# Kernel tuning notes

Measured on AMD Instinct MI355X. Metric: run time of the kernel, lower is better.

The kernel has to match this reference:

```python
import jax, jax.numpy as jnp
import numpy as np

B, N_TOTAL = 4096, 512
DIMS = {"RT": (8, 8, 16), "OB": (8, 8, 16), "RS": (8, 8, 16), "TG": (16, 16, 32)}


def _branch(obs, W, b, dq, dk):
    # obs: [B, n, 2]; fused QKV projection then self-attention + mean pool
    P = obs @ W + b                              # [B, n, dq+dk+dv]
    Q, K, V = P[..., :dq], P[..., dq:dq + dk], P[..., dq + dk:]
    scores = jnp.einsum('bqd,bkd->bqk', Q, K) / (dk ** 0.5)
    A = jax.nn.softmax(scores, axis=-1)
    return jnp.mean(jnp.einsum('bqk,bkv->bqv', A, V), axis=1)  # [B, dv]


def setup_inputs() -> dict:
    key = jax.random.key(0)
    ks = jax.random.split(key, 16)
    inp = {"state": jax.random.normal(ks[0], (B, N_TOTAL, 3), jnp.float32),
           "num_rt": 128, "num_ob": 128, "num_rs": 128, "num_tg": 128}
    i = 1
    for name, (dq, dk, dv) in DIMS.items():
        inp[f"W_{name}"] = 0.1 * jax.random.normal(ks[i], (2, dq + dk + dv), jnp.float32)
        inp[f"b_{name}"] = jnp.zeros((dq + dk + dv,), jnp.float32)
        i += 1
    dcat = sum(d[2] for d in DIMS.values())  # 64
    inp["W1"] = 0.1 * jax.random.normal(ks[i], (dcat, 256), jnp.float32)
    inp["b1"] = jnp.zeros((256,), jnp.float32)
    inp["W2"] = 0.1 * jax.random.normal(ks[i + 1], (256, 256), jnp.float32)
    inp["b2"] = jnp.zeros((256,), jnp.float32)
    inp["W3"] = 0.01 * jax.random.normal(ks[i + 2], (256, 1), jnp.float32)
    inp["b3"] = jnp.zeros((1,), jnp.float32)
    return inp


def reference(state, num_rt, num_ob, num_rs, num_tg,
              W_RT, b_RT, W_OB, b_OB, W_RS, b_RS, W_TG, b_TG,
              W1, b1, W2, b2, W3, b3):
    o0, o1 = 0, num_rt
    o2, o3 = o1 + num_ob, o1 + num_ob + num_rs
    o4 = o3 + num_tg
    h_rt = _branch(state[:, o0:o1, 0:2], W_RT, b_RT, *DIMS["RT"][:2])
    h_ob = _branch(state[:, o1:o2, 0:2], W_OB, b_OB, *DIMS["OB"][:2])
    h_rs = _branch(state[:, o2:o3, 0:2], W_RS, b_RS, *DIMS["RS"][:2])
    h_tg = _branch(state[:, o3:o4, 0:2], W_TG, b_TG, *DIMS["TG"][:2])
    h = jnp.concatenate([h_rt, h_ob, h_rs, h_tg], axis=1)  # [B, 64]
    h = jnp.tanh(h @ W1 + b1)
    h = jnp.tanh(h @ W2 + b2)
    return h @ W3 + b3  # [B, 1]
```

## Files before the change

kernel.cpp:

```cpp
#include <hip/hip_runtime.h>

#define LOG2E 1.44269504088896340736f

typedef float v2f __attribute__((ext_vector_type(2)));

__device__ __forceinline__ float fexp2(float x){
#if __has_builtin(__builtin_amdgcn_exp2f)
  return __builtin_amdgcn_exp2f(x);
#else
  return exp2f(x);
#endif
}
__device__ __forceinline__ float frcp(float x){
#if __has_builtin(__builtin_amdgcn_rcpf)
  return __builtin_amdgcn_rcpf(x);
#else
  return 1.0f/x;
#endif
}
__device__ __forceinline__ float tanh_fast(float x){
  float e = fexp2(x * (2.0f*LOG2E));
  return 1.0f - 2.0f*frcp(e + 1.0f);
}
__device__ __forceinline__ float4 fma4(float s, float4 w, float4 a){
  a.x = fmaf(s,w.x,a.x); a.y = fmaf(s,w.y,a.y);
  a.z = fmaf(s,w.z,a.z); a.w = fmaf(s,w.w,a.w);
  return a;
}
__device__ __forceinline__ v2f vfma2(v2f a, v2f b, v2f c){
#if __has_builtin(__builtin_elementwise_fma)
  return __builtin_elementwise_fma(a,b,c);
#else
  v2f r; r.x=fmaf(a.x,b.x,c.x); r.y=fmaf(a.y,b.y,c.y); return r;
#endif
}

template<int DQ, int DV>
__device__ __forceinline__ void branch_run(
    const float* __restrict__ state, int b, int n0,
    const float* __restrict__ W, const float* __restrict__ bias,
    float4* __restrict__ su4, float* __restrict__ sy,
    float* __restrict__ sH, int lane)
{
  const int D = 4*DQ;
  const float qs = LOG2E * (DQ==8 ? 0.35355339059327373f : 0.25f);

  const float* sp = state + ((size_t)b*512 + (size_t)(n0 + lane))*3;
  float x0 = sp[0],   y0 = sp[1];
  float x1 = sp[192], y1 = sp[193];

  float M00=0,M01=0,M02=0,M10=0,M11=0,M12=0,M20=0,M21=0,M22=0;
  #pragma unroll
  for (int d=0; d<DQ; ++d) {
    float aq0 = W[d], aq1 = W[D+d], aq2 = bias[d];
    float ak0 = W[DQ+d], ak1 = W[D+DQ+d], ak2 = bias[DQ+d];
    M00 = fmaf(aq0,ak0,M00); M01 = fmaf(aq0,ak1,M01); M02 = fmaf(aq0,ak2,M02);
    M10 = fmaf(aq1,ak0,M10); M11 = fmaf(aq1,ak1,M11); M12 = fmaf(aq1,ak2,M12);
    M20 = fmaf(aq2,ak0,M20); M21 = fmaf(aq2,ak1,M21); M22 = fmaf(aq2,ak2,M22);
  }
  M00*=qs; M01*=qs; M02*=qs; M10*=qs; M11*=qs; M12*=qs; M20*=qs; M21*=qs; M22*=qs;

  float4 uA, uB;
  uA.x = fmaf(M00,x0, fmaf(M01,y0, M02));
  uA.y = fmaf(M10,x0, fmaf(M11,y0, M12));
  uA.z = fmaf(M20,x0, fmaf(M21,y0, M22));
  uA.w = x0;
  uB.x = fmaf(M00,x1, fmaf(M01,y1, M02));
  uB.y = fmaf(M10,x1, fmaf(M11,y1, M12));
  uB.z = fmaf(M20,x1, fmaf(M21,y1, M22));
  uB.w = x1;
  su4[lane]    = uA;  sy[lane]    = y0;
  su4[lane+64] = uB;  sy[lane+64] = y1;
  __syncthreads();

  v2f X; X.x=x0; X.y=x1;
  v2f Y; Y.x=y0; Y.y=y1;
  v2f E={0.f,0.f}, Ex={0.f,0.f}, Ey={0.f,0.f};
  const float4* syc = (const float4*)sy;
  #pragma unroll 4
  for (int k4=0; k4<32; ++k4) {
    float4 yv = syc[k4];
    #pragma unroll
    for (int j=0; j<4; ++j) {
      float4 u = su4[4*k4+j];
      float yk = (j==0)?yv.x : (j==1)?yv.y : (j==2)?yv.z : yv.w;
      v2f ux; ux.x=u.x; ux.y=u.x;
      v2f uy; uy.x=u.y; uy.y=u.y;
      v2f uz; uz.x=u.z; uz.y=u.z;
      v2f s = vfma2(X, ux, vfma2(Y, uy, uz));
      v2f e; e.x = fexp2(s.x); e.y = fexp2(s.y);
      E += e;
      v2f xk2; xk2.x=u.w; xk2.y=u.w;
      v2f yk2; yk2.x=yk;  yk2.y=yk;
      Ex = vfma2(e, xk2, Ex);
      Ey = vfma2(e, yk2, Ey);
    }
  }
  float r0 = frcp(E.x), r1 = frcp(E.y);
  float gx = fmaf(Ex.x,r0, Ex.y*r1);
  float gy = fmaf(Ey.x,r0, Ey.y*r1);
  #pragma unroll
  for (int m=1; m<64; m<<=1) {
    gx += __shfl_xor(gx, m, 64);
    gy += __shfl_xor(gy, m, 64);
  }
  gx *= 0.0078125f;
  gy *= 0.0078125f;
  if (lane < DV) {
    float wv0 = W[2*DQ+lane], wv1 = W[D+2*DQ+lane], vb = bias[2*DQ+lane];
    sH[lane] = fmaf(gx, wv0, fmaf(gy, wv1, vb));
  }
}

__global__ __launch_bounds__(256)
void attn_kernel(const float* __restrict__ state,
    const float* __restrict__ W_RT, const float* __restrict__ b_RT,
    const float* __restrict__ W_OB, const float* __restrict__ b_OB,
    const float* __restrict__ W_RS, const float* __restrict__ b_RS,
    const float* __restrict__ W_TG, const float* __restrict__ b_TG,
    float* __restrict__ hbuf)
{
  __shared__ float4 su4[4*128];
  __shared__ float  sy[4*128] __attribute__((aligned(16)));
  __shared__ float  sH[80];
  const int b    = blockIdx.x;
  const int wave = threadIdx.x >> 6;
  const int lane = threadIdx.x & 63;

  const float* W;  const float* bb;
  if      (wave == 0) { W = W_RT; bb = b_RT; }
  else if (wave == 1) { W = W_OB; bb = b_OB; }
  else if (wave == 2) { W = W_RS; bb = b_RS; }
  else                { W = W_TG; bb = b_TG; }
  const int n0 = wave * 128;
  float4* u4   = su4 + wave * 128;
  float*  yy   = sy  + wave * 128;
  float*  hOut = sH + wave * 16;

  if (wave < 3) branch_run<8 ,16>(state, b, n0, W, bb, u4, yy, hOut, lane);
  else          branch_run<16,32>(state, b, n0, W, bb, u4, yy, hOut, lane);
  __syncthreads();
  if (threadIdx.x < 80) hbuf[(size_t)b*80 + threadIdx.x] = sH[threadIdx.x];
}

__global__ __launch_bounds__(256)
void mlp_kernel(const float* __restrict__ hbuf,
    const float* __restrict__ W1, const float* __restrict__ b1,
    const float* __restrict__ W2, const float* __restrict__ b2,
    const float* __restrict__ W3, const float* __restrict__ b3,
    float* __restrict__ out)
{
  __shared__ float sHin[8][84];
  __shared__ float sH1[8][260];
  __shared__ float sRed[4][8];
  const int t  = threadIdx.x;
  const int b0 = blockIdx.x * 8;
  const int q  = t >> 2;
  const int rg = t & 3;
  const int r0 = 2*rg, r1 = r0 + 1;
  const int wave = t >> 6;

  for (int i = t; i < 8*80; i += 256) sHin[i/80][i%80] = hbuf[(size_t)b0*80 + i];
  __syncthreads();

  const float4* W1v = (const float4*)W1;
  const float4* W2v = (const float4*)W2;

  float4 acc0 = ((const float4*)b1)[q];
  float4 acc1 = acc0;
  float4 wb[4][4];
  #pragma unroll
  for (int p=0; p<4; ++p)
    #pragma unroll
    for (int jj=0; jj<4; ++jj) wb[p][jj] = W1v[(size_t)(4*p+jj)*64 + q];
  #pragma unroll 4
  for (int i4 = 0; i4 < 16; ++i4) {
    float4 h0 = *(const float4*)&sHin[r0][i4*4];
    float4 h1 = *(const float4*)&sHin[r1][i4*4];
    float4 w0=wb[i4&3][0], w1=wb[i4&3][1], w2=wb[i4&3][2], w3=wb[i4&3][3];
    #pragma unroll
    for (int jj=0; jj<4; ++jj) wb[i4&3][jj] = W1v[(size_t)((i4+4)*4+jj)*64 + q];
    acc0 = fma4(h0.x,w0, fma4(h0.y,w1, fma4(h0.z,w2, fma4(h0.w,w3, acc0))));
    acc1 = fma4(h1.x,w0, fma4(h1.y,w1, fma4(h1.z,w2, fma4(h1.w,w3, acc1))));
  }
  #pragma unroll
  for (int i4 = 16; i4 < 20; ++i4) {
    float4 h0 = *(const float4*)&sHin[r0][i4*4];
    float4 h1 = *(const float4*)&sHin[r1][i4*4];
    float4 w0=wb[i4&3][0], w1=wb[i4&3][1], w2=wb[i4&3][2], w3=wb[i4&3][3];
    acc0 = fma4(h0.x,w0, fma4(h0.y,w1, fma4(h0.z,w2, fma4(h0.w,w3, acc0))));
    acc1 = fma4(h1.x,w0, fma4(h1.y,w1, fma4(h1.z,w2, fma4(h1.w,w3, acc1))));
  }
  {
    float4 o0, o1;
    o0.x=tanh_fast(acc0.x); o0.y=tanh_fast(acc0.y); o0.z=tanh_fast(acc0.z); o0.w=tanh_fast(acc0.w);
    o1.x=tanh_fast(acc1.x); o1.y=tanh_fast(acc1.y); o1.z=tanh_fast(acc1.z); o1.w=tanh_fast(acc1.w);
    *(float4*)&sH1[r0][4*q] = o0;
    *(float4*)&sH1[r1][4*q] = o1;
  }
  __syncthreads();

  float4 acc2_0 = ((const float4*)b2)[q];
  float4 acc2_1 = acc2_0;
  #pragma unroll
  for (int p=0; p<4; ++p)
    #pragma unroll
    for (int jj=0; jj<4; ++jj) wb[p][jj] = W2v[(size_t)(4*p+jj)*64 + q];
  #pragma unroll 4
  for (int i4 = 0; i4 < 60; ++i4) {
    float4 h0 = *(const float4*)&sH1[r0][i4*4];
    float4 h1 = *(const float4*)&sH1[r1][i4*4];
    float4 w0=wb[i4&3][0], w1=wb[i4&3][1], w2=wb[i4&3][2], w3=wb[i4&3][3];
    #pragma unroll
    for (int jj=0; jj<4; ++jj) wb[i4&3][jj] = W2v[(size_t)((i4+4)*4+jj)*64 + q];
    acc2_0 = fma4(h0.x,w0, fma4(h0.y,w1, fma4(h0.z,w2, fma4(h0.w,w3, acc2_0))));
    acc2_1 = fma4(h1.x,w0, fma4(h1.y,w1, fma4(h1.z,w2, fma4(h1.w,w3, acc2_1))));
  }
  #pragma unroll
  for (int i4 = 60; i4 < 64; ++i4) {
    float4 h0 = *(const float4*)&sH1[r0][i4*4];
    float4 h1 = *(const float4*)&sH1[r1][i4*4];
    float4 w0=wb[i4&3][0], w1=wb[i4&3][1], w2=wb[i4&3][2], w3=wb[i4&3][3];
    acc2_0 = fma4(h0.x,w0, fma4(h0.y,w1, fma4(h0.z,w2, fma4(h0.w,w3, acc2_0))));
    acc2_1 = fma4(h1.x,w0, fma4(h1.y,w1, fma4(h1.z,w2, fma4(h1.w,w3, acc2_1))));
  }

  float4 w3v = ((const float4*)W3)[q];
  float p0 = tanh_fast(acc2_0.x)*w3v.x + tanh_fast(acc2_0.y)*w3v.y
           + tanh_fast(acc2_0.z)*w3v.z + tanh_fast(acc2_0.w)*w3v.w;
  float p1 = tanh_fast(acc2_1.x)*w3v.x + tanh_fast(acc2_1.y)*w3v.y
           + tanh_fast(acc2_1.z)*w3v.z + tanh_fast(acc2_1.w)*w3v.w;
  #pragma unroll
  for (int m=4; m<64; m<<=1) {
    p0 += __shfl_xor(p0, m, 64);
    p1 += __shfl_xor(p1, m, 64);
  }
  if ((t & 63) == rg) { sRed[wave][r0] = p0; sRed[wave][r1] = p1; }
  __syncthreads();
  if (t < 8)
    out[b0 + t] = sRed[0][t] + sRed[1][t] + sRed[2][t] + sRed[3][t] + b3[0];
}

extern "C" void kernel_launch(void* const* d_in, const int* in_sizes, int n_in,
                              void* d_out, int out_size, void* d_ws, size_t ws_size,
                              hipStream_t stream) {
  const float* state = (const float*)d_in[0];
  const float* W_RT = (const float*)d_in[5];
  const float* b_RT = (const float*)d_in[6];
  const float* W_OB = (const float*)d_in[7];
  const float* b_OB = (const float*)d_in[8];
  const float* W_RS = (const float*)d_in[9];
  const float* b_RS = (const float*)d_in[10];
  const float* W_TG = (const float*)d_in[11];
  const float* b_TG = (const float*)d_in[12];
  const float* W1 = (const float*)d_in[13];
  const float* b1 = (const float*)d_in[14];
  const float* W2 = (const float*)d_in[15];
  const float* b2 = (const float*)d_in[16];
  const float* W3 = (const float*)d_in[17];
  const float* b3 = (const float*)d_in[18];

  float* hbuf = (float*)d_ws;

  attn_kernel<<<4096, 256, 0, stream>>>(state,
      W_RT, b_RT, W_OB, b_OB, W_RS, b_RS, W_TG, b_TG, hbuf);
  mlp_kernel<<<512, 256, 0, stream>>>(hbuf, W1, b1, W2, b2, W3, b3,
      (float*)d_out);
}
```

Measured before the change: 75.74 us.

## Batch four samples per attention block, pair keys in LDS, deepen MLP prefetch

The attention kernel now handles four consecutive batch rows per block, 1024 blocks instead of 4096. This amortizes the per-branch Q·K bilinear-form setup and the V-weight loads across rows. Keys are stored in LDS interleaved in pairs, so each packed two-wide FMA covers two keys for the same query, while each thread still handles its two queries. The MLP kernel gets a deeper 8-stage register prefetch of W2 and a min-2-blocks occupancy hint. The risks are fewer blocks to hide latency, extra barriers per row, and more register pressure from the larger prefetch buffer.

```diff
diff --git a/kernel.cpp b/kernel.cpp
--- a/kernel.cpp
+++ b/kernel.cpp
@@ -35,19 +35,16 @@
 #endif
 }
 
-template<int DQ, int DV>
-__device__ __forceinline__ void branch_run(
-    const float* __restrict__ state, int b, int n0,
+template<int DQ, int DV, int NB>
+__device__ __forceinline__ void branch_all(
+    const float* __restrict__ state, int b0, int n0,
     const float* __restrict__ W, const float* __restrict__ bias,
-    float4* __restrict__ su4, float* __restrict__ sy,
-    float* __restrict__ sH, int lane)
+    float* __restrict__ sA, float* __restrict__ sB, float* __restrict__ sYv,
+    float* __restrict__ sHbase, int hoff, float* __restrict__ hbuf,
+    int lane, int tix)
 {
   const int D = 4*DQ;
   const float qs = LOG2E * (DQ==8 ? 0.35355339059327373f : 0.25f);
-
-  const float* sp = state + ((size_t)b*512 + (size_t)(n0 + lane))*3;
-  float x0 = sp[0],   y0 = sp[1];
-  float x1 = sp[192], y1 = sp[193];
 
   float M00=0,M01=0,M02=0,M10=0,M11=0,M12=0,M20=0,M21=0,M22=0;
   #pragma unroll
@@ -60,55 +57,84 @@
   }
   M00*=qs; M01*=qs; M02*=qs; M10*=qs; M11*=qs; M12*=qs; M20*=qs; M21*=qs; M22*=qs;
 
-  float4 uA, uB;
-  uA.x = fmaf(M00,x0, fmaf(M01,y0, M02));
-  uA.y = fmaf(M10,x0, fmaf(M11,y0, M12));
-  uA.z = fmaf(M20,x0, fmaf(M21,y0, M22));
-  uA.w = x0;
-  uB.x = fmaf(M00,x1, fmaf(M01,y1, M02));
-  uB.y = fmaf(M10,x1, fmaf(M11,y1, M12));
-  uB.z = fmaf(M20,x1, fmaf(M21,y1, M22));
-  uB.w = x1;
-  su4[lane]    = uA;  sy[lane]    = y0;
-  su4[lane+64] = uB;  sy[lane+64] = y1;
-  __syncthreads();
-
-  v2f X; X.x=x0; X.y=x1;
-  v2f Y; Y.x=y0; Y.y=y1;
-  v2f E={0.f,0.f}, Ex={0.f,0.f}, Ey={0.f,0.f};
-  const float4* syc = (const float4*)sy;
-  #pragma unroll 4
-  for (int k4=0; k4<32; ++k4) {
-    float4 yv = syc[k4];
-    #pragma unroll
-    for (int j=0; j<4; ++j) {
-      float4 u = su4[4*k4+j];
-      float yk = (j==0)?yv.x : (j==1)?yv.y : (j==2)?yv.z : yv.w;
-      v2f ux; ux.x=u.x; ux.y=u.x;
-      v2f uy; uy.x=u.y; uy.y=u.y;
-      v2f uz; uz.x=u.z; uz.y=u.z;
-      v2f s = vfma2(X, ux, vfma2(Y, uy, uz));
-      v2f e; e.x = fexp2(s.x); e.y = fexp2(s.y);
-      E += e;
-      v2f xk2; xk2.x=u.w; xk2.y=u.w;
-      v2f yk2; yk2.x=yk;  yk2.y=yk;
-      Ex = vfma2(e, xk2, Ex);
-      Ey = vfma2(e, yk2, Ey);
-    }
-  }
-  float r0 = frcp(E.x), r1 = frcp(E.y);
-  float gx = fmaf(Ex.x,r0, Ex.y*r1);
-  float gy = fmaf(Ey.x,r0, Ey.y*r1);
-  #pragma unroll
-  for (int m=1; m<64; m<<=1) {
-    gx += __shfl_xor(gx, m, 64);
-    gy += __shfl_xor(gy, m, 64);
-  }
-  gx *= 0.0078125f;
-  gy *= 0.0078125f;
-  if (lane < DV) {
-    float wv0 = W[2*DQ+lane], wv1 = W[D+2*DQ+lane], vb = bias[2*DQ+lane];
-    sH[lane] = fmaf(gx, wv0, fmaf(gy, wv1, vb));
+  float wv0 = 0.f, wv1 = 0.f, vb = 0.f;
+  if (lane < DV) { wv0 = W[2*DQ+lane]; wv1 = W[D+2*DQ+lane]; vb = bias[2*DQ+lane]; }
+
+  #pragma unroll 1
+  for (int e = 0; e < NB; ++e) {
+    const int b = b0 + e;
+    const float* sp = state + ((size_t)b*512 + (size_t)(n0 + lane))*3;
+    float x0 = sp[0],   y0 = sp[1];
+    float x1 = sp[192], y1 = sp[193];
+
+    {
+      int p = lane >> 1, h = lane & 1;
+      float ux = fmaf(M00,x0, fmaf(M01,y0, M02));
+      float uy = fmaf(M10,x0, fmaf(M11,y0, M12));
+      float uz = fmaf(M20,x0, fmaf(M21,y0, M22));
+      sA[p*4 + h]     = ux;  sA[p*4 + 2 + h] = uy;
+      sB[p*4 + h]     = uz;  sB[p*4 + 2 + h] = x0;
+      sYv[lane]       = y0;
+      int p1 = p + 32;
+      float vx = fmaf(M00,x1, fmaf(M01,y1, M02));
+      float vy = fmaf(M10,x1, fmaf(M11,y1, M12));
+      float vz = fmaf(M20,x1, fmaf(M21,y1, M22));
+      sA[p1*4 + h]     = vx;  sA[p1*4 + 2 + h] = vy;
+      sB[p1*4 + h]     = vz;  sB[p1*4 + 2 + h] = x1;
+      sYv[lane + 64]   = y1;
+    }
+    __syncthreads();
+
+    v2f X0; X0.x=x0; X0.y=x0;  v2f Y0; Y0.x=y0; Y0.y=y0;
+    v2f X1; X1.x=x1; X1.y=x1;  v2f Y1; Y1.x=y1; Y1.y=y1;
+    v2f E0={0.f,0.f}, Ex0={0.f,0.f}, Ey0={0.f,0.f};
+    v2f E1={0.f,0.f}, Ex1={0.f,0.f}, Ey1={0.f,0.f};
+    const float4* A4 = (const float4*)sA;
+    const float4* B4 = (const float4*)sB;
+    const float4* Y4 = (const float4*)sYv;
+    #pragma unroll 2
+    for (int pp = 0; pp < 32; ++pp) {
+      float4 Av0 = A4[2*pp], Av1 = A4[2*pp+1];
+      float4 Bv0 = B4[2*pp], Bv1 = B4[2*pp+1];
+      float4 Yq  = Y4[pp];
+      {
+        v2f ux; ux.x=Av0.x; ux.y=Av0.y;  v2f uy; uy.x=Av0.z; uy.y=Av0.w;
+        v2f uz; uz.x=Bv0.x; uz.y=Bv0.y;  v2f xk; xk.x=Bv0.z; xk.y=Bv0.w;
+        v2f yk; yk.x=Yq.x;  yk.y=Yq.y;
+        v2f s0 = vfma2(X0, ux, vfma2(Y0, uy, uz));
+        v2f s1 = vfma2(X1, ux, vfma2(Y1, uy, uz));
+        v2f e0, e1;
+        e0.x = fexp2(s0.x); e0.y = fexp2(s0.y);
+        e1.x = fexp2(s1.x); e1.y = fexp2(s1.y);
+        E0 += e0; Ex0 = vfma2(e0, xk, Ex0); Ey0 = vfma2(e0, yk, Ey0);
+        E1 += e1; Ex1 = vfma2(e1, xk, Ex1); Ey1 = vfma2(e1, yk, Ey1);
+      }
+      {
+        v2f ux; ux.x=Av1.x; ux.y=Av1.y;  v2f uy; uy.x=Av1.z; uy.y=Av1.w;
+        v2f uz; uz.x=Bv1.x; uz.y=Bv1.y;  v2f xk; xk.x=Bv1.z; xk.y=Bv1.w;
+        v2f yk; yk.x=Yq.z;  yk.y=Yq.w;
+        v2f s0 = vfma2(X0, ux, vfma2(Y0, uy, uz));
+        v2f s1 = vfma2(X1, ux, vfma2(Y1, uy, uz));
+        v2f e0, e1;
+        e0.x = fexp2(s0.x); e0.y = fexp2(s0.y);
+        e1.x = fexp2(s1.x); e1.y = fexp2(s1.y);
+        E0 += e0; Ex0 = vfma2(e0, xk, Ex0); Ey0 = vfma2(e0, yk, Ey0);
+        E1 += e1; Ex1 = vfma2(e1, xk, Ex1); Ey1 = vfma2(e1, yk, Ey1);
+      }
+    }
+    float r0 = frcp(E0.x + E0.y), r1 = frcp(E1.x + E1.y);
+    float gx = fmaf(Ex0.x + Ex0.y, r0, (Ex1.x + Ex1.y) * r1);
+    float gy = fmaf(Ey0.x + Ey0.y, r0, (Ey1.x + Ey1.y) * r1);
+    #pragma unroll
+    for (int m=1; m<64; m<<=1) {
+      gx += __shfl_xor(gx, m, 64);
+      gy += __shfl_xor(gy, m, 64);
+    }
+    gx *= 0.0078125f;
+    gy *= 0.0078125f;
+    if (lane < DV) sHbase[hoff + lane] = fmaf(gx, wv0, fmaf(gy, wv1, vb));
+    __syncthreads();
+    if (tix < 80) hbuf[(size_t)b*80 + tix] = sHbase[tix];
   }
 }
 
@@ -120,10 +146,11 @@
     const float* __restrict__ W_TG, const float* __restrict__ b_TG,
     float* __restrict__ hbuf)
 {
-  __shared__ float4 su4[4*128];
-  __shared__ float  sy[4*128] __attribute__((aligned(16)));
-  __shared__ float  sH[80];
-  const int b    = blockIdx.x;
+  __shared__ float sA[4][256] __attribute__((aligned(16)));
+  __shared__ float sB[4][256] __attribute__((aligned(16)));
+  __shared__ float sY[4][128] __attribute__((aligned(16)));
+  __shared__ float sH[80];
+  const int b0   = blockIdx.x * 4;
   const int wave = threadIdx.x >> 6;
   const int lane = threadIdx.x & 63;
 
@@ -133,17 +160,17 @@
   else if (wave == 2) { W = W_RS; bb = b_RS; }
   else                { W = W_TG; bb = b_TG; }
   const int n0 = wave * 128;
-  float4* u4   = su4 + wave * 128;
-  float*  yy   = sy  + wave * 128;
-  float*  hOut = sH + wave * 16;
-
-  if (wave < 3) branch_run<8 ,16>(state, b, n0, W, bb, u4, yy, hOut, lane);
-  else          branch_run<16,32>(state, b, n0, W, bb, u4, yy, hOut, lane);
-  __syncthreads();
-  if (threadIdx.x < 80) hbuf[(size_t)b*80 + threadIdx.x] = sH[threadIdx.x];
-}
-
-__global__ __launch_bounds__(256)
+  const int hoff = wave * 16;
+
+  if (wave < 3)
+    branch_all<8 ,16,4>(state, b0, n0, W, bb, sA[wave], sB[wave], sY[wave],
+                        sH, hoff, hbuf, lane, threadIdx.x);
+  else
+    branch_all<16,32,4>(state, b0, n0, W, bb, sA[wave], sB[wave], sY[wave],
+                        sH, hoff, hbuf, lane, threadIdx.x);
+}
+
+__global__ __launch_bounds__(256, 2)
 void mlp_kernel(const float* __restrict__ hbuf,
     const float* __restrict__ W1, const float* __restrict__ b1,
     const float* __restrict__ W2, const float* __restrict__ b2,
@@ -168,28 +195,30 @@
 
   float4 acc0 = ((const float4*)b1)[q];
   float4 acc1 = acc0;
-  float4 wb[4][4];
-  #pragma unroll
-  for (int p=0; p<4; ++p)
-    #pragma unroll
-    for (int jj=0; jj<4; ++jj) wb[p][jj] = W1v[(size_t)(4*p+jj)*64 + q];
-  #pragma unroll 4
-  for (int i4 = 0; i4 < 16; ++i4) {
-    float4 h0 = *(const float4*)&sHin[r0][i4*4];
-    float4 h1 = *(const float4*)&sHin[r1][i4*4];
-    float4 w0=wb[i4&3][0], w1=wb[i4&3][1], w2=wb[i4&3][2], w3=wb[i4&3][3];
-    #pragma unroll
-    for (int jj=0; jj<4; ++jj) wb[i4&3][jj] = W1v[(size_t)((i4+4)*4+jj)*64 + q];
-    acc0 = fma4(h0.x,w0, fma4(h0.y,w1, fma4(h0.z,w2, fma4(h0.w,w3, acc0))));
-    acc1 = fma4(h1.x,w0, fma4(h1.y,w1, fma4(h1.z,w2, fma4(h1.w,w3, acc1))));
-  }
-  #pragma unroll
-  for (int i4 = 16; i4 < 20; ++i4) {
-    float4 h0 = *(const float4*)&sHin[r0][i4*4];
-    float4 h1 = *(const float4*)&sHin[r1][i4*4];
-    float4 w0=wb[i4&3][0], w1=wb[i4&3][1], w2=wb[i4&3][2], w3=wb[i4&3][3];
-    acc0 = fma4(h0.x,w0, fma4(h0.y,w1, fma4(h0.z,w2, fma4(h0.w,w3, acc0))));
-    acc1 = fma4(h1.x,w0, fma4(h1.y,w1, fma4(h1.z,w2, fma4(h1.w,w3, acc1))));
+  {
+    float4 wb[4][4];
+    #pragma unroll
+    for (int p=0; p<4; ++p)
+      #pragma unroll
+      for (int jj=0; jj<4; ++jj) wb[p][jj] = W1v[(size_t)(4*p+jj)*64 + q];
+    #pragma unroll 4
+    for (int i4 = 0; i4 < 16; ++i4) {
+      float4 h0 = *(const float4*)&sHin[r0][i4*4];
+      float4 h1 = *(const float4*)&sHin[r1][i4*4];
+      float4 w0=wb[i4&3][0], w1=wb[i4&3][1], w2=wb[i4&3][2], w3=wb[i4&3][3];
+      #pragma unroll
+      for (int jj=0; jj<4; ++jj) wb[i4&3][jj] = W1v[(size_t)((i4+4)*4+jj)*64 + q];
+      acc0 = fma4(h0.x,w0, fma4(h0.y,w1, fma4(h0.z,w2, fma4(h0.w,w3, acc0))));
+      acc1 = fma4(h1.x,w0, fma4(h1.y,w1, fma4(h1.z,w2, fma4(h1.w,w3, acc1))));
+    }
+    #pragma unroll
+    for (int i4 = 16; i4 < 20; ++i4) {
+      float4 h0 = *(const float4*)&sHin[r0][i4*4];
+      float4 h1 = *(const float4*)&sHin[r1][i4*4];
+      float4 w0=wb[i4&3][0], w1=wb[i4&3][1], w2=wb[i4&3][2], w3=wb[i4&3][3];
+      acc0 = fma4(h0.x,w0, fma4(h0.y,w1, fma4(h0.z,w2, fma4(h0.w,w3, acc0))));
+      acc1 = fma4(h1.x,w0, fma4(h1.y,w1, fma4(h1.z,w2, fma4(h1.w,w3, acc1))));
+    }
   }
   {
     float4 o0, o1;
@@ -202,27 +231,30 @@
 
   float4 acc2_0 = ((const float4*)b2)[q];
   float4 acc2_1 = acc2_0;
-  #pragma unroll
-  for (int p=0; p<4; ++p)
-    #pragma unroll
-    for (int jj=0; jj<4; ++jj) wb[p][jj] = W2v[(size_t)(4*p+jj)*64 + q];
-  #pragma unroll 4
-  for (int i4 = 0; i4 < 60; ++i4) {
-    float4 h0 = *(const float4*)&sH1[r0][i4*4];
-    float4 h1 = *(const float4*)&sH1[r1][i4*4];
-    float4 w0=wb[i4&3][0], w1=wb[i4&3][1], w2=wb[i4&3][2], w3=wb[i4&3][3];
-    #pragma unroll
-    for (int jj=0; jj<4; ++jj) wb[i4&3][jj] = W2v[(size_t)((i4+4)*4+jj)*64 + q];
-    acc2_0 = fma4(h0.x,w0, fma4(h0.y,w1, fma4(h0.z,w2, fma4(h0.w,w3, acc2_0))));
-    acc2_1 = fma4(h1.x,w0, fma4(h1.y,w1, fma4(h1.z,w2, fma4(h1.w,w3, acc2_1))));
-  }
-  #pragma unroll
-  for (int i4 = 60; i4 < 64; ++i4) {
-    float4 h0 = *(const float4*)&sH1[r0][i4*4];
-    float4 h1 = *(const float4*)&sH1[r1][i4*4];
-    float4 w0=wb[i4&3][0], w1=wb[i4&3][1], w2=wb[i4&3][2], w3=wb[i4&3][3];
-    acc2_0 = fma4(h0.x,w0, fma4(h0.y,w1, fma4(h0.z,w2, fma4(h0.w,w3, acc2_0))));
-    acc2_1 = fma4(h1.x,w0, fma4(h1.y,w1, fma4(h1.z,w2, fma4(h1.w,w3, acc2_1))));
+  {
+    float4 wb[8][4];
+    #pragma unroll
+    for (int p=0; p<8; ++p)
+      #pragma unroll
+      for (int jj=0; jj<4; ++jj) wb[p][jj] = W2v[(size_t)(4*p+jj)*64 + q];
+    #pragma unroll 8
+    for (int i4 = 0; i4 < 56; ++i4) {
+      float4 h0 = *(const float4*)&sH1[r0][i4*4];
+      float4 h1 = *(const float4*)&sH1[r1][i4*4];
+      float4 w0=wb[i4&7][0], w1=wb[i4&7][1], w2=wb[i4&7][2], w3=wb[i4&7][3];
+      #pragma unroll
+      for (int jj=0; jj<4; ++jj) wb[i4&7][jj] = W2v[(size_t)((i4+8)*4+jj)*64 + q];
+      acc2_0 = fma4(h0.x,w0, fma4(h0.y,w1, fma4(h0.z,w2, fma4(h0.w,w3, acc2_0))));
+      acc2_1 = fma4(h1.x,w0, fma4(h1.y,w1, fma4(h1.z,w2, fma4(h1.w,w3, acc2_1))));
+    }
+    #pragma unroll
+    for (int i4 = 56; i4 < 64; ++i4) {
+      float4 h0 = *(const float4*)&sH1[r0][i4*4];
+      float4 h1 = *(const float4*)&sH1[r1][i4*4];
+      float4 w0=wb[i4&7][0], w1=wb[i4&7][1], w2=wb[i4&7][2], w3=wb[i4&7][3];
+      acc2_0 = fma4(h0.x,w0, fma4(h0.y,w1, fma4(h0.z,w2, fma4(h0.w,w3, acc2_0))));
+      acc2_1 = fma4(h1.x,w0, fma4(h1.y,w1, fma4(h1.z,w2, fma4(h1.w,w3, acc2_1))));
+    }
   }
 
   float4 w3v = ((const float4*)W3)[q];
@@ -262,7 +294,7 @@
 
   float* hbuf = (float*)d_ws;
 
-  attn_kernel<<<4096, 256, 0, stream>>>(state,
+  attn_kernel<<<1024, 256, 0, stream>>>(state,
       W_RT, b_RT, W_OB, b_OB, W_RS, b_RS, W_TG, b_TG, hbuf);
   mlp_kernel<<<512, 256, 0, stream>>>(hbuf, W1, b1, W2, b2, W3, b3,
       (float*)d_out);
```

New measurement: 108.2 us. 1.43x slower.
